# Optimization experiments

Hardware: AMD Instinct MI355X
Metric: run time of the kernel (lower is better)

The kernel has to match this reference:

```python
import jax, jax.numpy as jnp
import numpy as np

BS, L, D = 128, 256, 512
H, DK = 2, 256  # heads, head dim
EPS_BN = 1e-5


def _lin(x, W, b):
    # torch Linear: W is (out, in)
    return jnp.einsum('...i,oi->...o', x, W) + b


def _bn(x, g, b, m, v):
    # eval-mode BatchNorm over channel axis = last axis of x
    return (x - m) * (g * jax.lax.rsqrt(v + EPS_BN)) + b


def setup_inputs() -> dict:
    key = jax.random.key(0)
    ks = iter(jax.random.split(key, 64))
    rn = lambda shape, s=0.02: jax.random.normal(next(ks), shape, dtype=jnp.float32) * s
    inp = {}
    inp['cap_emb'] = jax.random.normal(next(ks), (BS, L, D), dtype=jnp.float32)
    inp['lengths'] = jax.random.randint(next(ks), (BS,), 1, L + 1, dtype=jnp.int64 if jax.config.jax_enable_x64 else jnp.int32)
    # GA linears q,k,v
    for nm in ('Wq', 'Wk', 'Wv'):
        inp[nm] = rn((D, D))
    for nm in ('bq', 'bk', 'bv'):
        inp[nm] = rn((D,))
    inp['Wfq'] = rn((DK, DK)); inp['bfq'] = rn((DK,))
    inp['Wfk'] = rn((DK, DK)); inp['bfk'] = rn((DK,))
    inp['Wfg'] = rn((2 * DK, DK)); inp['bfg'] = rn((2 * DK,))
    # BatchNorm params (eval running stats)
    for pre in ('bn1', 'bn2', 'bn3'):
        inp[pre + '_g'] = 1.0 + rn((D,), 0.1)
        inp[pre + '_b'] = rn((D,), 0.1)
        inp[pre + '_m'] = rn((D,), 0.1)
        inp[pre + '_v'] = jax.random.uniform(next(ks), (D,), minval=0.5, maxval=1.5, dtype=jnp.float32)
    # Conv1d weights, torch layout (out, in, k)
    inp['Wc2'] = rn((D, D, 2)); inp['bc2'] = rn((D,))
    inp['Wc3'] = rn((D, D, 3)); inp['bc3'] = rn((D,))
    # MLP 512 -> 1024 -> 512
    inp['Wm1'] = rn((2 * D, D)); inp['bm1'] = rn((2 * D,))
    inp['Wm2'] = rn((D, 2 * D)); inp['bm2'] = rn((D,))
    return inp


def _forward(cap_emb, Wq, bq, Wk, bk, Wv, bv, Wfq, bfq, Wfk, bfk, Wfg, bfg,
             bn1_g, bn1_b, bn1_m, bn1_v, Wc2, bc2, bn2_g, bn2_b, bn2_m, bn2_v,
             Wc3, bc3, bn3_g, bn3_b, bn3_m, bn3_v, Wm1, bm1, Wm2, bm2, lengths):
    bs, seq, dim = cap_emb.shape
    # ---- GA: gated self-attention ----
    def split_heads(x):
        return x.reshape(bs, seq, H, DK).transpose(0, 2, 1, 3)  # [bs,h,seq,dk]
    q = split_heads(_lin(cap_emb, Wq, bq))
    k = split_heads(_lin(cap_emb, Wk, bk))
    v = split_heads(_lin(cap_emb, Wv, bv))
    G = _lin(q, Wfq, bfq) * _lin(k, Wfk, bfk)
    M = jax.nn.sigmoid(_lin(G, Wfg, bfg))  # [bs,h,seq,2*dk]
    qg = q * M[..., :DK]
    kg = k * M[..., DK:]
    # torch.div(..., rounding_mode='floor') == elementwise floor of scaled scores
    scores = jnp.floor(jnp.einsum('bhqd,bhkd->bhqk', qg, kg) / jnp.sqrt(jnp.float32(DK)))
    p_attn = jax.nn.softmax(scores, axis=-1)
    x = jnp.einsum('bhqk,bhkd->bhqd', p_attn, v)
    x = x.transpose(0, 2, 1, 3).reshape(bs, seq, dim)
    # BN over features (eval), dropout is identity in eval mode
    ga_emb = cap_emb + _bn(x, bn1_g, bn1_b, bn1_m, bn1_v)
    # ---- dual conv1d branches ----
    xc = cap_emb.transpose(0, 2, 1)  # [bs, D, L]
    dn = ('NCW', 'OIW', 'NCW')
    c2 = jax.lax.conv_general_dilated(xc, Wc2, window_strides=(2,), padding='VALID', dimension_numbers=dn) + bc2[None, :, None]
    c3 = jax.lax.conv_general_dilated(xc, Wc3, window_strides=(3,), padding='VALID', dimension_numbers=dn) + bc3[None, :, None]
    f2 = jax.nn.relu(_bn(c2.transpose(0, 2, 1), bn2_g, bn2_b, bn2_m, bn2_v))
    f3 = jax.nn.relu(_bn(c3.transpose(0, 2, 1), bn3_g, bn3_b, bn3_m, bn3_v))
    ga_jw = jnp.concatenate([ga_emb, f2, f3], axis=1)
    # ---- residual MLP (dropout identity in eval) ----
    hid = jax.nn.relu(_lin(ga_jw, Wm1, bm1))
    tex_emb = _lin(hid, Wm2, bm2) + ga_jw
    # ---- length-indexed gather ----
    idx = lengths.astype(jnp.int32) - 1
    out = tex_emb[jnp.arange(bs), idx]  # [bs, D]
    # l2norm
    norm = jnp.sqrt(jnp.sum(out * out, axis=-1, keepdims=True)) + 1e-8
    return out / norm


def reference(cap_emb, lengths, Wq, bq, Wk, bk, Wv, bv, Wfq, bfq, Wfk, bfk, Wfg, bfg,
              bn1_g, bn1_b, bn1_m, bn1_v, Wc2, bc2, bn2_g, bn2_b, bn2_m, bn2_v,
              Wc3, bc3, bn3_g, bn3_b, bn3_m, bn3_v, Wm1, bm1, Wm2, bm2):
    return _forward(cap_emb, Wq, bq, Wk, bk, Wv, bv, Wfq, bfq, Wfk, bfk, Wfg, bfg,
                    bn1_g, bn1_b, bn1_m, bn1_v, Wc2, bc2, bn2_g, bn2_b, bn2_m, bn2_v,
                    Wc3, bc3, bn3_g, bn3_b, bn3_m, bn3_v, Wm1, bm1, Wm2, bm2, lengths)
```

## Files before the change

### kernel.cpp

```cpp
#include <hip/hip_runtime.h>
#include <math.h>


typedef short bf16x8 __attribute__((ext_vector_type(8)));
typedef float f32x4 __attribute__((ext_vector_type(4)));
typedef short short4v __attribute__((ext_vector_type(4)));

__device__ __forceinline__ short f2bf(float x) {
    union { float f; unsigned u; } c; c.f = x;
    unsigned r = c.u + 0x7FFFu + ((c.u >> 16) & 1u);
    return (short)(r >> 16);
}
__device__ __forceinline__ float bf2f(short h) {
    union { float f; unsigned u; } c; c.u = ((unsigned)(unsigned short)h) << 16;
    return c.f;
}
__device__ __forceinline__ void glds16(const void* g, void* l) {
    __builtin_amdgcn_global_load_lds(
        (const __attribute__((address_space(1))) void*)g,
        (__attribute__((address_space(3))) void*)l, 16, 0, 0);
}

struct CastArgs {
    const float* src[4];
    short* dst[4];
    int n4[4];
};
__global__ __launch_bounds__(256) void cast_multi(CastArgs a)
{
    const int j = blockIdx.y;
    const float4* s = (const float4*)a.src[j];
    short* d = a.dst[j];
    const int n4 = a.n4[j];
    for (int i = blockIdx.x * 256 + threadIdx.x; i < n4; i += gridDim.x * 256) {
        float4 x = s[i];
        short4v h;
        h.x = f2bf(x.x); h.y = f2bf(x.y); h.z = f2bf(x.z); h.w = f2bf(x.w);
        *(short4v*)&d[i * 4] = h;
    }
}

__global__ __launch_bounds__(256)
void compose(const float* __restrict__ Wq, const float* __restrict__ bq,
             const float* __restrict__ Wfq, const float* __restrict__ bfq,
             short* __restrict__ WaHi, float* __restrict__ ba)
{
    __shared__ float fq[256];
    __shared__ float redc[256];
    const int op = blockIdx.x;
    const int h = op >> 8, o = op & 255;
    const int t = threadIdx.x;
    fq[t] = Wfq[o * 256 + t];
    redc[t] = fq[t] * bq[h * 256 + t];
    __syncthreads();
    for (int s = 128; s > 0; s >>= 1) {
        if (t < s) redc[t] += redc[t + s];
        __syncthreads();
    }
    if (t == 0) ba[op] = redc[0] + bfq[o];
    float s0 = 0.f, s1 = 0.f;
    for (int d = 0; d < 256; ++d) {
        const float f = fq[d];
        const float* wr = Wq + (size_t)(h * 256 + d) * 512;
        s0 += f * wr[t];
        s1 += f * wr[t + 256];
    }
    const size_t ro = (size_t)op * 512;
    WaHi[ro + t] = f2bf(s0);
    WaHi[ro + 256 + t] = f2bf(s1);
}

__device__ __forceinline__ void kloop_1p(
    const short* __restrict__ A, int lda,
    const short* __restrict__ B, int ldb,
    int K, int bm, int bn, short (*lds)[8192], int tid, f32x4 acc[4][4])
{
    const int lane = tid & 63;
    const int wr = (tid >> 7) & 1, wc = (tid >> 6) & 1;
    const int fr = lane & 15, kc = lane >> 4;
    const int r0 = tid >> 2;
    const int e0 = (((tid & 3) ^ ((r0 >> 1) & 3))) * 8;
    const int kce = (kc ^ ((fr >> 1) & 3)) * 8;

    auto stage = [&](int ph, int k0) {
        short* b = lds[ph];
        glds16(A + (size_t)(bm + r0) * lda + k0 + e0,      b + tid * 8);
        glds16(A + (size_t)(bm + r0 + 64) * lda + k0 + e0, b + (tid + 256) * 8);
        glds16(B + (size_t)(bn + r0) * ldb + k0 + e0,      b + 4096 + tid * 8);
        glds16(B + (size_t)(bn + r0 + 64) * ldb + k0 + e0, b + 4096 + (tid + 256) * 8);
    };

    stage(0, 0);
    __syncthreads();
    const int NS = K / 32;
    for (int s = 0; s < NS; ++s) {
        if (s + 1 < NS) stage((s + 1) & 1, (s + 1) * 32);
        const short* b = lds[s & 1];
        bf16x8 ah[4], bh[4];
#pragma unroll
        for (int i = 0; i < 4; ++i)
            ah[i] = *(const bf16x8*)&b[(wr * 64 + i * 16 + fr) * 32 + kce];
#pragma unroll
        for (int i = 0; i < 4; ++i)
            bh[i] = *(const bf16x8*)&b[4096 + (wc * 64 + i * 16 + fr) * 32 + kce];
#pragma unroll
        for (int mi = 0; mi < 4; ++mi)
#pragma unroll
            for (int ni = 0; ni < 4; ++ni)
                acc[mi][ni] = __builtin_amdgcn_mfma_f32_16x16x32_bf16(ah[mi], bh[ni], acc[mi][ni], 0, 0, 0);
        __syncthreads();
    }
}

__global__ __launch_bounds__(256, 2)
void gemm_k1(const short* __restrict__ capB, const short* __restrict__ WkB,
             const float* __restrict__ bk, short* __restrict__ Kbuf)
{
    __shared__ short lds[2][8192];
    const int tid = threadIdx.x;
    const int bm = blockIdx.y * 128;
    const int bn = blockIdx.x * 128;

    f32x4 acc[4][4];
#pragma unroll
    for (int i = 0; i < 4; ++i)
#pragma unroll
        for (int j = 0; j < 4; ++j) acc[i][j] = (f32x4){0.f, 0.f, 0.f, 0.f};

    kloop_1p(capB, 512, WkB, 512, 512, bm, bn, lds, tid, acc);

    const int lane = tid & 63;
    const int wr = (tid >> 7) & 1, wc = (tid >> 6) & 1;
    const int fr = lane & 15, kc = lane >> 4;
#pragma unroll
    for (int mi = 0; mi < 4; ++mi) {
#pragma unroll
        for (int ni = 0; ni < 4; ++ni) {
#pragma unroll
            for (int r = 0; r < 4; ++r) {
                const int row = bm + wr * 64 + mi * 16 + kc * 4 + r;
                const int col = bn + wc * 64 + ni * 16 + fr;
                Kbuf[(size_t)row * 512 + col] = f2bf(acc[mi][ni][r] + bk[col]);
            }
        }
    }
}

__global__ __launch_bounds__(256, 2)
void gemm_g(const short* __restrict__ Kbuf,
            const short* __restrict__ capB,
            const short* __restrict__ WfkB, const short* __restrict__ WaB,
            const float* __restrict__ bfk, const float* __restrict__ ba,
            short* __restrict__ Gbuf)
{
    __shared__ short lds[2][8192];
    const int tid = threadIdx.x;
    const int bm = blockIdx.y * 128;
    const int bn = blockIdx.x * 128;
    const int z = blockIdx.z;

    f32x4 acc1[4][4], acc2[4][4];
#pragma unroll
    for (int i = 0; i < 4; ++i)
#pragma unroll
        for (int j = 0; j < 4; ++j) {
            acc1[i][j] = (f32x4){0.f, 0.f, 0.f, 0.f};
            acc2[i][j] = (f32x4){0.f, 0.f, 0.f, 0.f};
        }

    kloop_1p(Kbuf + (size_t)z * 256, 512, WfkB, 256, 256, bm, bn, lds, tid, acc1);
    kloop_1p(capB, 512, WaB + (size_t)z * 256 * 512, 512, 512, bm, bn, lds, tid, acc2);

    const int lane = tid & 63;
    const int wr = (tid >> 7) & 1, wc = (tid >> 6) & 1;
    const int fr = lane & 15, kc = lane >> 4;
#pragma unroll
    for (int mi = 0; mi < 4; ++mi) {
#pragma unroll
        for (int ni = 0; ni < 4; ++ni) {
#pragma unroll
            for (int r = 0; r < 4; ++r) {
                const int row = bm + wr * 64 + mi * 16 + kc * 4 + r;
                const int col = bn + wc * 64 + ni * 16 + fr;
                const float lin = acc1[mi][ni][r] + bfk[col];
                const float av  = acc2[mi][ni][r] + ba[z * 256 + col];
                Gbuf[(size_t)row * 512 + z * 256 + col] = f2bf(lin * av);
            }
        }
    }
}

__global__ __launch_bounds__(256, 2)
void gemm_kg(const short* __restrict__ Gbuf,
             const short* __restrict__ Wfg2B, const float* __restrict__ bias,
             const short* __restrict__ Kbuf,
             const float* __restrict__ qg, float* __restrict__ scorep)
{
    __shared__ short lds[2][8192];
    __shared__ float sp[256];
    const int tid = threadIdx.x;
    const int bm = blockIdx.y * 128;
    const int bn = blockIdx.x * 128;
    const int z = blockIdx.z;

    f32x4 acc[4][4];
#pragma unroll
    for (int i = 0; i < 4; ++i)
#pragma unroll
        for (int j = 0; j < 4; ++j) acc[i][j] = (f32x4){0.f, 0.f, 0.f, 0.f};

    kloop_1p(Gbuf + (size_t)z * 256, 512, Wfg2B, 256, 256, bm, bn, lds, tid, acc);

    const int lane = tid & 63;
    const int wr = (tid >> 7) & 1, wc = (tid >> 6) & 1;
    const int fr = lane & 15, kc = lane >> 4;

    float qgv[4];
    float pt[4][4];
    {
        const int b = bm >> 8;
#pragma unroll
        for (int ni = 0; ni < 4; ++ni)
            qgv[ni] = qg[b * 512 + z * 256 + bn + wc * 64 + ni * 16 + fr];
#pragma unroll
        for (int mi = 0; mi < 4; ++mi)
#pragma unroll
            for (int r = 0; r < 4; ++r) pt[mi][r] = 0.f;
    }

#pragma unroll
    for (int mi = 0; mi < 4; ++mi) {
#pragma unroll
        for (int ni = 0; ni < 4; ++ni) {
#pragma unroll
            for (int r = 0; r < 4; ++r) {
                const int row = bm + wr * 64 + mi * 16 + kc * 4 + r;
                const int col = bn + wc * 64 + ni * 16 + fr;
                const float v = acc[mi][ni][r] + bias[col];
                const float e = bf2f(Kbuf[(size_t)row * 512 + z * 256 + col]);
                const float kgv = e / (1.f + expf(-v));
                pt[mi][r] += kgv * qgv[ni];
            }
        }
    }

#pragma unroll
    for (int mi = 0; mi < 4; ++mi) {
#pragma unroll
        for (int r = 0; r < 4; ++r) {
            float p = pt[mi][r];
            p += __shfl_xor(p, 1);
            p += __shfl_xor(p, 2);
            p += __shfl_xor(p, 4);
            p += __shfl_xor(p, 8);
            if (fr == 0) {
                const int row_local = wr * 64 + mi * 16 + kc * 4 + r;
                sp[row_local * 2 + wc] = p;
            }
        }
    }
    __syncthreads();
    if (tid < 128) {
        const int row = bm + tid;
        const float s = sp[tid * 2] + sp[tid * 2 + 1];
        const int b = row >> 8, j = row & 255;
        scorep[((size_t)(b * 2 + z) * 256 + j) * 2 + blockIdx.x] = s;
    }
}

__global__ __launch_bounds__(256)
void qg_kernel(const float* __restrict__ cap,
               const short* __restrict__ Gbuf,
               const float* __restrict__ Wq, const float* __restrict__ bq,
               const float* __restrict__ Wfg, const float* __restrict__ bfg,
               const int* __restrict__ lengths, float* __restrict__ qg)
{
    __shared__ float cr[512];
    __shared__ float gs[256];
    const int b = blockIdx.x >> 1, h = blockIdx.x & 1;
    const int t = threadIdx.x;
    int r = lengths[b] - 1;
    if (r < 0) r = 0;
    if (r > 255) r = 255;
    const size_t base = ((size_t)b * 256 + r) * 512;
    cr[t] = cap[base + t];
    cr[t + 256] = cap[base + 256 + t];
    gs[t] = bf2f(Gbuf[base + h * 256 + t]);
    __syncthreads();
    const float4* wq4 = (const float4*)(Wq + (size_t)(h * 256 + t) * 512);
    float q = 0.f;
    for (int k4 = 0; k4 < 128; ++k4) {
        float4 w = wq4[k4];
        q += w.x * cr[k4 * 4 + 0] + w.y * cr[k4 * 4 + 1]
           + w.z * cr[k4 * 4 + 2] + w.w * cr[k4 * 4 + 3];
    }
    q += bq[h * 256 + t];
    const float4* w4 = (const float4*)(Wfg + (size_t)t * 256);
    float a = 0.f;
    for (int k4 = 0; k4 < 64; ++k4) {
        float4 w = w4[k4];
        a += w.x * gs[k4 * 4 + 0] + w.y * gs[k4 * 4 + 1]
           + w.z * gs[k4 * 4 + 2] + w.w * gs[k4 * 4 + 3];
    }
    a += bfg[t];
    qg[b * 512 + h * 256 + t] = q / (1.f + expf(-a));
}

__global__ __launch_bounds__(256)
void pbar_kernel(const float* __restrict__ scorep, const short* __restrict__ capB,
                 float* __restrict__ pbar)
{
    __shared__ float sc[512], red[512];
    const int b = blockIdx.y, cg = blockIdx.x;
    const int t = threadIdx.x;
#pragma unroll
    for (int i = 0; i < 2; ++i) {
        const int o = t + i * 256;
        const int h = o >> 8, j = o & 255;
        const size_t si = ((size_t)(b * 2 + h) * 256 + j) * 2;
        sc[o] = floorf((scorep[si] + scorep[si + 1]) * 0.0625f);
    }
    __syncthreads();
    red[t] = sc[t]; red[t + 256] = sc[t + 256];
    __syncthreads();
    for (int s = 128; s > 0; s >>= 1) {
        if (t < s) {
            red[t] = fmaxf(red[t], red[t + s]);
            red[256 + t] = fmaxf(red[256 + t], red[256 + t + s]);
        }
        __syncthreads();
    }
    const float mx0 = red[0], mx1 = red[256];
    __syncthreads();
    const float e0 = expf(sc[t] - mx0);
    const float e1 = expf(sc[t + 256] - mx1);
    red[t] = e0; red[t + 256] = e1;
    __syncthreads();
    for (int s = 128; s > 0; s >>= 1) {
        if (t < s) { red[t] += red[t + s]; red[256 + t] += red[256 + t + s]; }
        __syncthreads();
    }
    sc[t] = e0 / red[0];
    sc[t + 256] = e1 / red[256];
    __syncthreads();

    const int c = cg * 64 + (t & 63);
    const int jg = t >> 6;
    float a0 = 0.f, a1 = 0.f;
    for (int j = jg * 64; j < jg * 64 + 64; ++j) {
        const float cv = bf2f(capB[((size_t)(b * 256 + j)) * 512 + c]);
        a0 += sc[j] * cv;
        a1 += sc[256 + j] * cv;
    }
    red[t] = a0;
    __syncthreads();
    if (t < 64) {
        const float s0 = red[t] + red[t + 64] + red[t + 128] + red[t + 192];
        pbar[b * 1024 + cg * 64 + t] = s0;
    }
    __syncthreads();
    red[t] = a1;
    __syncthreads();
    if (t < 64) {
        const float s1 = red[t] + red[t + 64] + red[t + 128] + red[t + 192];
        pbar[b * 1024 + 512 + cg * 64 + t] = s1;
    }
}

__global__ __launch_bounds__(256)
void bnx_kernel(const float* __restrict__ pbar, const float* __restrict__ cap,
                const int* __restrict__ lengths,
                const float* __restrict__ Wv, const float* __restrict__ bv,
                const float* __restrict__ g1, const float* __restrict__ b1,
                const float* __restrict__ m1, const float* __restrict__ v1,
                float* __restrict__ xga)
{
    __shared__ float pb[1024];
    const int b = blockIdx.x;
    const int t = threadIdx.x;
    int r = lengths[b] - 1;
    if (r < 0) r = 0;
    if (r > 255) r = 255;
    const size_t base = ((size_t)b * 256 + r) * 512;
    pb[t] = pbar[b * 1024 + t];
    pb[t + 256] = pbar[b * 1024 + 256 + t];
    pb[t + 512] = pbar[b * 1024 + 512 + t];
    pb[t + 768] = pbar[b * 1024 + 768 + t];
    __syncthreads();
    float x0 = 0.f, x1 = 0.f;
    {
        const float4* w4 = (const float4*)(Wv + (size_t)t * 512);
        for (int k4 = 0; k4 < 128; ++k4) {
            float4 w = w4[k4];
            x0 += w.x * pb[k4 * 4 + 0] + w.y * pb[k4 * 4 + 1]
                + w.z * pb[k4 * 4 + 2] + w.w * pb[k4 * 4 + 3];
        }
        x0 += bv[t];
    }
    {
        const float4* w4 = (const float4*)(Wv + (size_t)(t + 256) * 512);
        for (int k4 = 0; k4 < 128; ++k4) {
            float4 w = w4[k4];
            x1 += w.x * pb[512 + k4 * 4 + 0] + w.y * pb[512 + k4 * 4 + 1]
                + w.z * pb[512 + k4 * 4 + 2] + w.w * pb[512 + k4 * 4 + 3];
        }
        x1 += bv[t + 256];
    }
    const int c0 = t, c1 = t + 256;
    const float s0 = g1[c0] / sqrtf(v1[c0] + 1e-5f);
    const float s1 = g1[c1] / sqrtf(v1[c1] + 1e-5f);
    xga[b * 512 + c0] = cap[base + c0] + (x0 - m1[c0]) * s0 + b1[c0];
    xga[b * 512 + c1] = cap[base + c1] + (x1 - m1[c1]) * s1 + b1[c1];
}

__global__ __launch_bounds__(256)
void mlp1(const float* __restrict__ xga, const float* __restrict__ W,
          const float* __restrict__ bias, float* __restrict__ hid)
{
    __shared__ float xs[16 * 512];
    const int r0 = blockIdx.y * 16;
    const int c0 = blockIdx.x * 64;
    for (int i = threadIdx.x; i < 2048; i += 256)
        ((float4*)xs)[i] = ((const float4*)(xga + (size_t)r0 * 512))[i];
    __syncthreads();
    const int col = c0 + (threadIdx.x & 63);
    const int rg = (threadIdx.x >> 6) * 4;
    float acc[4] = {0.f, 0.f, 0.f, 0.f};
    const float4* w4 = (const float4*)(W + (size_t)col * 512);
    for (int k4 = 0; k4 < 128; ++k4) {
        float4 w = w4[k4];
#pragma unroll
        for (int rr = 0; rr < 4; ++rr) {
            float4 x = *(const float4*)&xs[(rg + rr) * 512 + k4 * 4];
            acc[rr] += w.x * x.x + w.y * x.y + w.z * x.z + w.w * x.w;
        }
    }
    const float bb = bias[col];
#pragma unroll
    for (int rr = 0; rr < 4; ++rr)
        hid[(size_t)(r0 + rg + rr) * 1024 + col] = fmaxf(acc[rr] + bb, 0.f);
}

__global__ __launch_bounds__(256)
void mlp2(const float* __restrict__ hid, const float* __restrict__ W,
          const float* __restrict__ bias, const float* __restrict__ xga,
          float* __restrict__ tex)
{
    __shared__ float xs[16 * 1024];
    const int r0 = blockIdx.y * 16;
    const int c0 = blockIdx.x * 64;
    for (int i = threadIdx.x; i < 4096; i += 256)
        ((float4*)xs)[i] = ((const float4*)(hid + (size_t)r0 * 1024))[i];
    __syncthreads();
    const int col = c0 + (threadIdx.x & 63);
    const int rg = (threadIdx.x >> 6) * 4;
    float acc[4] = {0.f, 0.f, 0.f, 0.f};
    const float4* w4 = (const float4*)(W + (size_t)col * 1024);
    for (int k4 = 0; k4 < 256; ++k4) {
        float4 w = w4[k4];
#pragma unroll
        for (int rr = 0; rr < 4; ++rr) {
            float4 x = *(const float4*)&xs[(rg + rr) * 1024 + k4 * 4];
            acc[rr] += w.x * x.x + w.y * x.y + w.z * x.z + w.w * x.w;
        }
    }
    const float bb = bias[col];
#pragma unroll
    for (int rr = 0; rr < 4; ++rr) {
        const int row = r0 + rg + rr;
        tex[(size_t)row * 512 + col] = acc[rr] + bb + xga[(size_t)row * 512 + col];
    }
}

__global__ __launch_bounds__(256)
void norm_out(const float* __restrict__ tex, float* __restrict__ out)
{
    __shared__ float red[256];
    const int b = blockIdx.x;
    const int t = threadIdx.x;
    const float a = tex[b * 512 + t];
    const float c = tex[b * 512 + 256 + t];
    red[t] = a * a + c * c;
    __syncthreads();
    for (int s = 128; s > 0; s >>= 1) {
        if (t < s) red[t] += red[t + s];
        __syncthreads();
    }
    const float inv = 1.f / (sqrtf(red[0]) + 1e-8f);
    out[b * 512 + t] = a * inv;
    out[b * 512 + 256 + t] = c * inv;
}

extern "C" void kernel_launch(void* const* d_in, const int* in_sizes, int n_in,
                              void* d_out, int out_size, void* d_ws, size_t ws_size,
                              hipStream_t stream)
{
    const float* cap = (const float*)d_in[0];
    const int* lengths = (const int*)d_in[1];
    const float* Wq  = (const float*)d_in[2];
    const float* Wk  = (const float*)d_in[3];
    const float* Wv  = (const float*)d_in[4];
    const float* bq  = (const float*)d_in[5];
    const float* bk  = (const float*)d_in[6];
    const float* bv  = (const float*)d_in[7];
    const float* Wfq = (const float*)d_in[8];
    const float* bfq = (const float*)d_in[9];
    const float* Wfk = (const float*)d_in[10];
    const float* bfk = (const float*)d_in[11];
    const float* Wfg = (const float*)d_in[12];
    const float* bfg = (const float*)d_in[13];
    const float* g1  = (const float*)d_in[14];
    const float* b1  = (const float*)d_in[15];
    const float* m1  = (const float*)d_in[16];
    const float* v1  = (const float*)d_in[17];
    const float* Wm1 = (const float*)d_in[30];
    const float* bm1 = (const float*)d_in[31];
    const float* Wm2 = (const float*)d_in[32];
    const float* bm2 = (const float*)d_in[33];
    float* out = (float*)d_out;

    char* w = (char*)d_ws;
    const size_t MB = 1024 * 1024;
    short* capB = (short*)(w);
    short* Kbuf = (short*)(w + 32 * MB);
    short* Gbuf = (short*)(w + 64 * MB);
    char* wp = w + 96 * MB;
    short* WkB   = (short*)wp; wp += 524288;
    short* WaB   = (short*)wp; wp += 524288;
    short* WfkB  = (short*)wp; wp += 131072;
    short* Wfg2B = (short*)wp; wp += 131072;
    float* ba     = (float*)wp; wp += 2048;
    float* qg     = (float*)wp; wp += 262144;
    float* scorep = (float*)wp; wp += 524288;
    float* pbar   = (float*)wp; wp += 524288;
    float* xga    = (float*)wp; wp += 262144;
    float* hid    = (float*)wp; wp += 524288;
    float* tex    = (float*)wp; wp += 262144;

    CastArgs ca;
    ca.src[0] = cap;          ca.dst[0] = capB;  ca.n4[0] = 4194304;
    ca.src[1] = Wk;           ca.dst[1] = WkB;   ca.n4[1] = 65536;
    ca.src[2] = Wfk;          ca.dst[2] = WfkB;  ca.n4[2] = 16384;
    ca.src[3] = Wfg + 65536;  ca.dst[3] = Wfg2B; ca.n4[3] = 16384;
    cast_multi<<<dim3(4096, 4), 256, 0, stream>>>(ca);

    compose<<<dim3(512), 256, 0, stream>>>(Wq, bq, Wfq, bfq, WaB, ba);

    gemm_k1<<<dim3(4, 256), 256, 0, stream>>>(capB, WkB, bk, Kbuf);

    gemm_g<<<dim3(2, 256, 2), 256, 0, stream>>>(Kbuf, capB, WfkB, WaB, bfk, ba, Gbuf);

    qg_kernel<<<dim3(256), 256, 0, stream>>>(cap, Gbuf, Wq, bq, Wfg, bfg, lengths, qg);

    gemm_kg<<<dim3(2, 256, 2), 256, 0, stream>>>(Gbuf, Wfg2B, bfg + 256, Kbuf, qg, scorep);

    pbar_kernel<<<dim3(8, 128), 256, 0, stream>>>(scorep, capB, pbar);
    bnx_kernel<<<dim3(128), 256, 0, stream>>>(pbar, cap, lengths, Wv, bv, g1, b1, m1, v1, xga);

    mlp1<<<dim3(16, 8), 256, 0, stream>>>(xga, Wm1, bm1, hid);
    mlp2<<<dim3(8, 8), 256, 0, stream>>>(hid, Wm2, bm2, xga, tex);
    norm_out<<<dim3(128), 256, 0, stream>>>(tex, out);
}
```

Before: 272.7 us.

## Fold Wfk into Wk weights and recompute K inside downstream GEMMs

```diff
diff --git a/kernel.cpp b/kernel.cpp
--- a/kernel.cpp
+++ b/kernel.cpp
@@ -22,9 +22,9 @@
 }
 
 struct CastArgs {
-    const float* src[4];
-    short* dst[4];
-    int n4[4];
+    const float* src[3];
+    short* dst[3];
+    int n4[3];
 };
 __global__ __launch_bounds__(256) void cast_multi(CastArgs a)
 {
@@ -41,33 +41,44 @@
 }
 
 __global__ __launch_bounds__(256)
-void compose(const float* __restrict__ Wq, const float* __restrict__ bq,
-             const float* __restrict__ Wfq, const float* __restrict__ bfq,
-             short* __restrict__ WaHi, float* __restrict__ ba)
+void compose2(const float* __restrict__ Wq, const float* __restrict__ bq,
+              const float* __restrict__ Wfq, const float* __restrict__ bfq,
+              const float* __restrict__ Wk, const float* __restrict__ bk,
+              const float* __restrict__ Wfk, const float* __restrict__ bfk,
+              short* __restrict__ WaB, float* __restrict__ ba,
+              short* __restrict__ WbB, float* __restrict__ bb)
 {
     __shared__ float fq[256];
     __shared__ float redc[256];
     const int op = blockIdx.x;
     const int h = op >> 8, o = op & 255;
     const int t = threadIdx.x;
-    fq[t] = Wfq[o * 256 + t];
-    redc[t] = fq[t] * bq[h * 256 + t];
+    const bool second = (blockIdx.y == 1);
+    const float* W  = second ? Wk  : Wq;
+    const float* bv = second ? bk  : bq;
+    const float* F  = second ? Wfk : Wfq;
+    const float* bf = second ? bfk : bfq;
+    short* WB   = second ? WbB : WaB;
+    float* bout = second ? bb  : ba;
+
+    fq[t] = F[o * 256 + t];
+    redc[t] = fq[t] * bv[h * 256 + t];
     __syncthreads();
     for (int s = 128; s > 0; s >>= 1) {
         if (t < s) redc[t] += redc[t + s];
         __syncthreads();
     }
-    if (t == 0) ba[op] = redc[0] + bfq[o];
+    if (t == 0) bout[op] = redc[0] + bf[o];
     float s0 = 0.f, s1 = 0.f;
     for (int d = 0; d < 256; ++d) {
         const float f = fq[d];
-        const float* wr = Wq + (size_t)(h * 256 + d) * 512;
+        const float* wr = W + (size_t)(h * 256 + d) * 512;
         s0 += f * wr[t];
         s1 += f * wr[t + 256];
     }
     const size_t ro = (size_t)op * 512;
-    WaHi[ro + t] = f2bf(s0);
-    WaHi[ro + 256 + t] = f2bf(s1);
+    WB[ro + t] = f2bf(s0);
+    WB[ro + 256 + t] = f2bf(s1);
 }
 
 __device__ __forceinline__ void kloop_1p(
@@ -113,51 +124,35 @@
 }
 
 __global__ __launch_bounds__(256, 2)
-void gemm_k1(const short* __restrict__ capB, const short* __restrict__ WkB,
-             const float* __restrict__ bk, short* __restrict__ Kbuf)
-{
-    __shared__ short lds[2][8192];
-    const int tid = threadIdx.x;
-    const int bm = blockIdx.y * 128;
-    const int bn = blockIdx.x * 128;
-
-    f32x4 acc[4][4];
-#pragma unroll
-    for (int i = 0; i < 4; ++i)
-#pragma unroll
-        for (int j = 0; j < 4; ++j) acc[i][j] = (f32x4){0.f, 0.f, 0.f, 0.f};
-
-    kloop_1p(capB, 512, WkB, 512, 512, bm, bn, lds, tid, acc);
-
-    const int lane = tid & 63;
-    const int wr = (tid >> 7) & 1, wc = (tid >> 6) & 1;
-    const int fr = lane & 15, kc = lane >> 4;
-#pragma unroll
-    for (int mi = 0; mi < 4; ++mi) {
-#pragma unroll
-        for (int ni = 0; ni < 4; ++ni) {
-#pragma unroll
-            for (int r = 0; r < 4; ++r) {
-                const int row = bm + wr * 64 + mi * 16 + kc * 4 + r;
-                const int col = bn + wc * 64 + ni * 16 + fr;
-                Kbuf[(size_t)row * 512 + col] = f2bf(acc[mi][ni][r] + bk[col]);
-            }
-        }
-    }
-}
-
-__global__ __launch_bounds__(256, 2)
-void gemm_g(const short* __restrict__ Kbuf,
-            const short* __restrict__ capB,
-            const short* __restrict__ WfkB, const short* __restrict__ WaB,
-            const float* __restrict__ bfk, const float* __restrict__ ba,
+void gemm_g(const short* __restrict__ capB,
+            const short* __restrict__ WaB, const short* __restrict__ WbB,
+            const float* __restrict__ ba, const float* __restrict__ bb,
             short* __restrict__ Gbuf)
 {
-    __shared__ short lds[2][8192];
+    __shared__ short lds[2][12288];
     const int tid = threadIdx.x;
     const int bm = blockIdx.y * 128;
     const int bn = blockIdx.x * 128;
     const int z = blockIdx.z;
+    const short* B1 = WaB + (size_t)z * 256 * 512;
+    const short* B2 = WbB + (size_t)z * 256 * 512;
+
+    const int lane = tid & 63;
+    const int wr = (tid >> 7) & 1, wc = (tid >> 6) & 1;
+    const int fr = lane & 15, kc = lane >> 4;
+    const int r0 = tid >> 2;
+    const int e0 = (((tid & 3) ^ ((r0 >> 1) & 3))) * 8;
+    const int kce = (kc ^ ((fr >> 1) & 3)) * 8;
+
+    auto stage = [&](int ph, int k0) {
+        short* b = lds[ph];
+        glds16(capB + (size_t)(bm + r0) * 512 + k0 + e0,      b + tid * 8);
+        glds16(capB + (size_t)(bm + r0 + 64) * 512 + k0 + e0, b + (tid + 256) * 8);
+        glds16(B1 + (size_t)(bn + r0) * 512 + k0 + e0,        b + 4096 + tid * 8);
+        glds16(B1 + (size_t)(bn + r0 + 64) * 512 + k0 + e0,   b + 4096 + (tid + 256) * 8);
+        glds16(B2 + (size_t)(bn + r0) * 512 + k0 + e0,        b + 8192 + tid * 8);
+        glds16(B2 + (size_t)(bn + r0 + 64) * 512 + k0 + e0,   b + 8192 + (tid + 256) * 8);
+    };
 
     f32x4 acc1[4][4], acc2[4][4];
 #pragma unroll
@@ -168,12 +163,34 @@
             acc2[i][j] = (f32x4){0.f, 0.f, 0.f, 0.f};
         }
 
-    kloop_1p(Kbuf + (size_t)z * 256, 512, WfkB, 256, 256, bm, bn, lds, tid, acc1);
-    kloop_1p(capB, 512, WaB + (size_t)z * 256 * 512, 512, 512, bm, bn, lds, tid, acc2);
-
-    const int lane = tid & 63;
-    const int wr = (tid >> 7) & 1, wc = (tid >> 6) & 1;
-    const int fr = lane & 15, kc = lane >> 4;
+    stage(0, 0);
+    __syncthreads();
+    for (int s = 0; s < 16; ++s) {
+        if (s + 1 < 16) stage((s + 1) & 1, (s + 1) * 32);
+        const short* b = lds[s & 1];
+        bf16x8 ah[4], bh[4];
+#pragma unroll
+        for (int i = 0; i < 4; ++i)
+            ah[i] = *(const bf16x8*)&b[(wr * 64 + i * 16 + fr) * 32 + kce];
+#pragma unroll
+        for (int i = 0; i < 4; ++i)
+            bh[i] = *(const bf16x8*)&b[4096 + (wc * 64 + i * 16 + fr) * 32 + kce];
+#pragma unroll
+        for (int mi = 0; mi < 4; ++mi)
+#pragma unroll
+            for (int ni = 0; ni < 4; ++ni)
+                acc1[mi][ni] = __builtin_amdgcn_mfma_f32_16x16x32_bf16(ah[mi], bh[ni], acc1[mi][ni], 0, 0, 0);
+#pragma unroll
+        for (int i = 0; i < 4; ++i)
+            bh[i] = *(const bf16x8*)&b[8192 + (wc * 64 + i * 16 + fr) * 32 + kce];
+#pragma unroll
+        for (int mi = 0; mi < 4; ++mi)
+#pragma unroll
+            for (int ni = 0; ni < 4; ++ni)
+                acc2[mi][ni] = __builtin_amdgcn_mfma_f32_16x16x32_bf16(ah[mi], bh[ni], acc2[mi][ni], 0, 0, 0);
+        __syncthreads();
+    }
+
 #pragma unroll
     for (int mi = 0; mi < 4; ++mi) {
 #pragma unroll
@@ -182,8 +199,8 @@
             for (int r = 0; r < 4; ++r) {
                 const int row = bm + wr * 64 + mi * 16 + kc * 4 + r;
                 const int col = bn + wc * 64 + ni * 16 + fr;
-                const float lin = acc1[mi][ni][r] + bfk[col];
-                const float av  = acc2[mi][ni][r] + ba[z * 256 + col];
+                const float av  = acc1[mi][ni][r] + ba[z * 256 + col];
+                const float lin = acc2[mi][ni][r] + bb[z * 256 + col];
                 Gbuf[(size_t)row * 512 + z * 256 + col] = f2bf(lin * av);
             }
         }
@@ -193,7 +210,8 @@
 __global__ __launch_bounds__(256, 2)
 void gemm_kg(const short* __restrict__ Gbuf,
              const short* __restrict__ Wfg2B, const float* __restrict__ bias,
-             const short* __restrict__ Kbuf,
+             const short* __restrict__ capB,
+             const short* __restrict__ WkB, const float* __restrict__ bk,
              const float* __restrict__ qg, float* __restrict__ scorep)
 {
     __shared__ short lds[2][8192];
@@ -203,13 +221,17 @@
     const int bn = blockIdx.x * 128;
     const int z = blockIdx.z;
 
-    f32x4 acc[4][4];
+    f32x4 acc1[4][4], acc2[4][4];
 #pragma unroll
     for (int i = 0; i < 4; ++i)
 #pragma unroll
-        for (int j = 0; j < 4; ++j) acc[i][j] = (f32x4){0.f, 0.f, 0.f, 0.f};
-
-    kloop_1p(Gbuf + (size_t)z * 256, 512, Wfg2B, 256, 256, bm, bn, lds, tid, acc);
+        for (int j = 0; j < 4; ++j) {
+            acc1[i][j] = (f32x4){0.f, 0.f, 0.f, 0.f};
+            acc2[i][j] = (f32x4){0.f, 0.f, 0.f, 0.f};
+        }
+
+    kloop_1p(Gbuf + (size_t)z * 256, 512, Wfg2B, 256, 256, bm, bn, lds, tid, acc1);
+    kloop_1p(capB, 512, WkB + (size_t)z * 256 * 512, 512, 512, bm, bn, lds, tid, acc2);
 
     const int lane = tid & 63;
     const int wr = (tid >> 7) & 1, wc = (tid >> 6) & 1;
@@ -234,10 +256,9 @@
         for (int ni = 0; ni < 4; ++ni) {
 #pragma unroll
             for (int r = 0; r < 4; ++r) {
-                const int row = bm + wr * 64 + mi * 16 + kc * 4 + r;
                 const int col = bn + wc * 64 + ni * 16 + fr;
-                const float v = acc[mi][ni][r] + bias[col];
-                const float e = bf2f(Kbuf[(size_t)row * 512 + z * 256 + col]);
+                const float v = acc1[mi][ni][r] + bias[col];
+                const float e = acc2[mi][ni][r] + bk[z * 256 + col];
                 const float kgv = e / (1.f + expf(-v));
                 pt[mi][r] += kgv * qgv[ni];
             }
@@ -522,14 +543,14 @@
     char* w = (char*)d_ws;
     const size_t MB = 1024 * 1024;
     short* capB = (short*)(w);
-    short* Kbuf = (short*)(w + 32 * MB);
-    short* Gbuf = (short*)(w + 64 * MB);
-    char* wp = w + 96 * MB;
+    short* Gbuf = (short*)(w + 32 * MB);
+    char* wp = w + 64 * MB;
     short* WkB   = (short*)wp; wp += 524288;
     short* WaB   = (short*)wp; wp += 524288;
-    short* WfkB  = (short*)wp; wp += 131072;
+    short* WbB   = (short*)wp; wp += 524288;
     short* Wfg2B = (short*)wp; wp += 131072;
     float* ba     = (float*)wp; wp += 2048;
+    float* bb     = (float*)wp; wp += 2048;
     float* qg     = (float*)wp; wp += 262144;
     float* scorep = (float*)wp; wp += 524288;
     float* pbar   = (float*)wp; wp += 524288;
@@ -540,19 +561,18 @@
     CastArgs ca;
     ca.src[0] = cap;          ca.dst[0] = capB;  ca.n4[0] = 4194304;
     ca.src[1] = Wk;           ca.dst[1] = WkB;   ca.n4[1] = 65536;
-    ca.src[2] = Wfk;          ca.dst[2] = WfkB;  ca.n4[2] = 16384;
-    ca.src[3] = Wfg + 65536;  ca.dst[3] = Wfg2B; ca.n4[3] = 16384;
-    cast_multi<<<dim3(4096, 4), 256, 0, stream>>>(ca);
-
-    compose<<<dim3(512), 256, 0, stream>>>(Wq, bq, Wfq, bfq, WaB, ba);
-
-    gemm_k1<<<dim3(4, 256), 256, 0, stream>>>(capB, WkB, bk, Kbuf);
-
-    gemm_g<<<dim3(2, 256, 2), 256, 0, stream>>>(Kbuf, capB, WfkB, WaB, bfk, ba, Gbuf);
+    ca.src[2] = Wfg + 65536;  ca.dst[2] = Wfg2B; ca.n4[2] = 16384;
+    cast_multi<<<dim3(4096, 3), 256, 0, stream>>>(ca);
+
+    compose2<<<dim3(512, 2), 256, 0, stream>>>(Wq, bq, Wfq, bfq, Wk, bk, Wfk, bfk,
+                                               WaB, ba, WbB, bb);
+
+    gemm_g<<<dim3(2, 256, 2), 256, 0, stream>>>(capB, WaB, WbB, ba, bb, Gbuf);
 
     qg_kernel<<<dim3(256), 256, 0, stream>>>(cap, Gbuf, Wq, bq, Wfg, bfg, lengths, qg);
 
-    gemm_kg<<<dim3(2, 256, 2), 256, 0, stream>>>(Gbuf, Wfg2B, bfg + 256, Kbuf, qg, scorep);
+    gemm_kg<<<dim3(2, 256, 2), 256, 0, stream>>>(Gbuf, Wfg2B, bfg + 256,
+                                                 capB, WkB, bk, qg, scorep);
 
     pbar_kernel<<<dim3(8, 128), 256, 0, stream>>>(scorep, capB, pbar);
     bnx_kernel<<<dim3(128), 256, 0, stream>>>(pbar, cap, lengths, Wv, bv, g1, b1, m1, v1, xga);
```

New measurement: 269.9 us. No clear change (-1.0%).
